# Kernel tuning notes

Measured on AMD Instinct MI355X. Metric: run time of the kernel, lower is better.

## Reference

```python
import jax, jax.numpy as jnp
import numpy as np

# Group structure (matches init_kwargs)
SIZES = np.array([16]*16 + [32]*32 + [64]*16)          # teacher_embedding_sizes_list
CHOICES = np.array([4]*16 + [8]*32 + [16]*16)          # max_choice_per_embedding
IN_DIM = int(SIZES.sum())                               # 2304
OUT_DIM = int(CHOICES.sum())                            # 576
W_TOTAL = int((SIZES * CHOICES).sum())                  # 25600
BATCH = 16384


def setup_inputs() -> dict:
    key = jax.random.key(0)
    k1, k2 = jax.random.split(key)
    x = jax.random.normal(k1, (BATCH, IN_DIM), dtype=jnp.float32)
    # TruncatedNormal(stddev=0.15) approximated with scaled normal
    weight = jax.random.normal(k2, (W_TOTAL, 1), dtype=jnp.float32) * 0.15
    bias = jnp.zeros((OUT_DIM,), dtype=jnp.float32)
    return {"x": x, "weight": weight, "bias": bias}


def reference(x, weight, bias):
    # Block-diagonal grouped GEMM: per-group slice of x times per-group weight
    # block reshaped to [size_i, choice_i], concatenated along features + bias.
    w_flat = weight[:, 0]
    outs = []
    w_idx = 0
    t_idx = 0
    for size, choice in zip(SIZES.tolist(), CHOICES.tolist()):
        x_slice = x[:, t_idx:t_idx + size]                       # [B, size]
        w_block = w_flat[w_idx:w_idx + size * choice].reshape(size, choice)
        outs.append(x_slice @ w_block)                           # [B, choice]
        w_idx += size * choice
        t_idx += size
    return jnp.concatenate(outs, axis=1) + bias
```

## Files before the change

kernel.cpp:

```cpp
#include <hip/hip_runtime.h>


#define BATCH   16384
#define IN_DIM  2304
#define OUT_DIM 576

template <int S, int C>
__global__ __launch_bounds__(256) void block_mm_kernel(
    const float* __restrict__ x, const float* __restrict__ w,
    const float* __restrict__ bias, float* __restrict__ out,
    int t_base, int o_base, int w_base)
{
    constexpr int W    = 4 * S;
    constexpr int LDSW = W + 4;
    __shared__ float xs[64 * LDSW];

    const int tid      = threadIdx.x;
    const int bg       = blockIdx.x;
    const int row_base = blockIdx.y * 64;

    const int x_col0 = t_base + bg * W;
    constexpr int VEC_PER_ROW = W / 4;
    constexpr int TOTAL_VEC   = 64 * VEC_PER_ROW;
    #pragma unroll
    for (int i = 0; i < TOTAL_VEC / 256; ++i) {
        const int f  = tid + 256 * i;
        const int r  = f / VEC_PER_ROW;
        const int c4 = f % VEC_PER_ROW;
        const float4 v = *reinterpret_cast<const float4*>(
            x + (size_t)(row_base + r) * IN_DIM + x_col0 + c4 * 4);
        *reinterpret_cast<float4*>(&xs[r * LDSW + c4 * 4]) = v;
    }
    __syncthreads();

    const int wid  = __builtin_amdgcn_readfirstlane(tid >> 6);
    const int lane = tid & 63;
    const int blk  = bg * 4 + wid;
    const float* __restrict__ wp = w + w_base + blk * (S * C);
    const int o_off = o_base + blk * C;

    float acc[C];
    #pragma unroll
    for (int c = 0; c < C; ++c) acc[c] = bias[o_off + c];

    const int xbase = lane * LDSW + wid * S;
    #pragma unroll
    for (int k4 = 0; k4 < S / 4; ++k4) {
        const float4 xv = *reinterpret_cast<const float4*>(&xs[xbase + k4 * 4]);
        #pragma unroll
        for (int j = 0; j < 4; ++j) {
            const float xj = j == 0 ? xv.x : j == 1 ? xv.y : j == 2 ? xv.z : xv.w;
            const int k = k4 * 4 + j;
            #pragma unroll
            for (int c = 0; c < C; ++c)
                acc[c] += xj * wp[k * C + c];
        }
    }

    float* __restrict__ op = out + (size_t)(row_base + lane) * OUT_DIM + o_off;
    #pragma unroll
    for (int c4 = 0; c4 < C / 4; ++c4) {
        const float4 v = make_float4(acc[c4 * 4 + 0], acc[c4 * 4 + 1],
                                     acc[c4 * 4 + 2], acc[c4 * 4 + 3]);
        *reinterpret_cast<float4*>(op + c4 * 4) = v;
    }
}

extern "C" void kernel_launch(void* const* d_in, const int* in_sizes, int n_in,
                              void* d_out, int out_size, void* d_ws, size_t ws_size,
                              hipStream_t stream) {
    const float* x    = (const float*)d_in[0];
    const float* w    = (const float*)d_in[1];
    const float* bias = (const float*)d_in[2];
    float* out        = (float*)d_out;

    const int row_tiles = BATCH / 64;

    block_mm_kernel<16, 4><<<dim3(4, row_tiles), 256, 0, stream>>>(
        x, w, bias, out, 0, 0, 0);
    block_mm_kernel<32, 8><<<dim3(8, row_tiles), 256, 0, stream>>>(
        x, w, bias, out, 256, 64, 1024);
    block_mm_kernel<64, 16><<<dim3(4, row_tiles), 256, 0, stream>>>(
        x, w, bias, out, 1280, 320, 9216);
}
```

Baseline: 243.0 us.

## Fuse three group kernels into one uniform 64x16 chunked block-diagonal kernel

Replaces the three templated launches with one kernel over 36 uniform chunks, each covering 64 input columns and 16 output columns per 64-row tile. Small groups are packed into dense 64x16 weight tiles in shared memory, padded with zeros off the block diagonal. Each wave computes 4 output columns using float4 LDS reads. This removes launch overhead and the per-thread global weight loads, and makes register use uniform. The cost is extra zero multiplies for the 16- and 32-wide groups and a per-block weight staging step.

```diff
diff --git a/kernel.cpp b/kernel.cpp
--- a/kernel.cpp
+++ b/kernel.cpp
@@ -4,66 +4,81 @@
 #define BATCH   16384
 #define IN_DIM  2304
 #define OUT_DIM 576
+#define CHUNKS  36
+#define XS_LDW  68
 
-template <int S, int C>
-__global__ __launch_bounds__(256) void block_mm_kernel(
+__global__ __launch_bounds__(256) void fused_block_mm(
     const float* __restrict__ x, const float* __restrict__ w,
-    const float* __restrict__ bias, float* __restrict__ out,
-    int t_base, int o_base, int w_base)
+    const float* __restrict__ bias, float* __restrict__ out)
 {
-    constexpr int W    = 4 * S;
-    constexpr int LDSW = W + 4;
-    __shared__ float xs[64 * LDSW];
+    __shared__ float xs[64 * XS_LDW];
+    __shared__ float wd[64 * 16];
 
-    const int tid      = threadIdx.x;
-    const int bg       = blockIdx.x;
-    const int row_base = blockIdx.y * 64;
+    const int tid = threadIdx.x;
+    const int bx  = blockIdx.x;
+    const int cj  = bx % CHUNKS;
+    const int rt  = bx / CHUNKS;
+    const int row_base = rt * 64;
 
-    const int x_col0 = t_base + bg * W;
-    constexpr int VEC_PER_ROW = W / 4;
-    constexpr int TOTAL_VEC   = 64 * VEC_PER_ROW;
+    if (cj < 4) {
+        const int wbase = cj * 256;
+        #pragma unroll
+        for (int i = 0; i < 4; ++i) {
+            const int e = tid + i * 256, k = e >> 4, c = e & 15, b = k >> 4;
+            wd[e] = ((c >> 2) == b)
+                  ? w[wbase + b * 64 + ((k & 15) << 2) + (c & 3)] : 0.0f;
+        }
+    } else if (cj < 20) {
+        const int wbase = 1024 + (cj - 4) * 512;
+        #pragma unroll
+        for (int i = 0; i < 4; ++i) {
+            const int e = tid + i * 256, k = e >> 4, c = e & 15, b = k >> 5;
+            wd[e] = ((c >> 3) == b)
+                  ? w[wbase + b * 256 + ((k & 31) << 3) + (c & 7)] : 0.0f;
+        }
+    } else {
+        const int wbase = 9216 + (cj - 20) * 1024;
+        #pragma unroll
+        for (int i = 0; i < 4; ++i) {
+            const int e = tid + i * 256;
+            wd[e] = w[wbase + e];
+        }
+    }
+
+    const float* __restrict__ xsrc = x + (size_t)row_base * IN_DIM + cj * 64;
     #pragma unroll
-    for (int i = 0; i < TOTAL_VEC / 256; ++i) {
-        const int f  = tid + 256 * i;
-        const int r  = f / VEC_PER_ROW;
-        const int c4 = f % VEC_PER_ROW;
+    for (int i = 0; i < 4; ++i) {
+        const int f = tid + i * 256, r = f >> 4, c = (f & 15) << 2;
         const float4 v = *reinterpret_cast<const float4*>(
-            x + (size_t)(row_base + r) * IN_DIM + x_col0 + c4 * 4);
-        *reinterpret_cast<float4*>(&xs[r * LDSW + c4 * 4]) = v;
+            xsrc + (size_t)r * IN_DIM + c);
+        *reinterpret_cast<float4*>(&xs[r * XS_LDW + c]) = v;
     }
     __syncthreads();
 
-    const int wid  = __builtin_amdgcn_readfirstlane(tid >> 6);
+    const int wv   = __builtin_amdgcn_readfirstlane(tid >> 6);
     const int lane = tid & 63;
-    const int blk  = bg * 4 + wid;
-    const float* __restrict__ wp = w + w_base + blk * (S * C);
-    const int o_off = o_base + blk * C;
+    const int ocol = cj * 16 + (wv << 2);
 
-    float acc[C];
+    float4 acc = make_float4(bias[ocol], bias[ocol + 1],
+                             bias[ocol + 2], bias[ocol + 3]);
+
+    const int xb = lane * XS_LDW;
+    const int wb = wv << 2;
     #pragma unroll
-    for (int c = 0; c < C; ++c) acc[c] = bias[o_off + c];
-
-    const int xbase = lane * LDSW + wid * S;
-    #pragma unroll
-    for (int k4 = 0; k4 < S / 4; ++k4) {
-        const float4 xv = *reinterpret_cast<const float4*>(&xs[xbase + k4 * 4]);
-        #pragma unroll
-        for (int j = 0; j < 4; ++j) {
-            const float xj = j == 0 ? xv.x : j == 1 ? xv.y : j == 2 ? xv.z : xv.w;
-            const int k = k4 * 4 + j;
-            #pragma unroll
-            for (int c = 0; c < C; ++c)
-                acc[c] += xj * wp[k * C + c];
-        }
+    for (int k4 = 0; k4 < 16; ++k4) {
+        const float4 xv = *reinterpret_cast<const float4*>(&xs[xb + (k4 << 2)]);
+        const float4 w0 = *reinterpret_cast<const float4*>(&wd[(k4*4+0)*16 + wb]);
+        const float4 w1 = *reinterpret_cast<const float4*>(&wd[(k4*4+1)*16 + wb]);
+        const float4 w2 = *reinterpret_cast<const float4*>(&wd[(k4*4+2)*16 + wb]);
+        const float4 w3 = *reinterpret_cast<const float4*>(&wd[(k4*4+3)*16 + wb]);
+        acc.x += xv.x*w0.x + xv.y*w1.x + xv.z*w2.x + xv.w*w3.x;
+        acc.y += xv.x*w0.y + xv.y*w1.y + xv.z*w2.y + xv.w*w3.y;
+        acc.z += xv.x*w0.z + xv.y*w1.z + xv.z*w2.z + xv.w*w3.z;
+        acc.w += xv.x*w0.w + xv.y*w1.w + xv.z*w2.w + xv.w*w3.w;
     }
 
-    float* __restrict__ op = out + (size_t)(row_base + lane) * OUT_DIM + o_off;
-    #pragma unroll
-    for (int c4 = 0; c4 < C / 4; ++c4) {
-        const float4 v = make_float4(acc[c4 * 4 + 0], acc[c4 * 4 + 1],
-                                     acc[c4 * 4 + 2], acc[c4 * 4 + 3]);
-        *reinterpret_cast<float4*>(op + c4 * 4) = v;
-    }
+    float* __restrict__ op = out + (size_t)(row_base + lane) * OUT_DIM + ocol;
+    *reinterpret_cast<float4*>(op) = acc;
 }
 
 extern "C" void kernel_launch(void* const* d_in, const int* in_sizes, int n_in,
@@ -75,11 +90,6 @@
     float* out        = (float*)d_out;
 
     const int row_tiles = BATCH / 64;
-
-    block_mm_kernel<16, 4><<<dim3(4, row_tiles), 256, 0, stream>>>(
-        x, w, bias, out, 0, 0, 0);
-    block_mm_kernel<32, 8><<<dim3(8, row_tiles), 256, 0, stream>>>(
-        x, w, bias, out, 256, 64, 1024);
-    block_mm_kernel<64, 16><<<dim3(4, row_tiles), 256, 0, stream>>>(
-        x, w, bias, out, 1280, 320, 9216);
+    fused_block_mm<<<dim3(CHUNKS * row_tiles), 256, 0, stream>>>(
+        x, w, bias, out);
 }
```

Measured after the change: 228.6 us. 1.06x faster.
